# Kernel tuning notes

Measured on AMD Instinct MI355X. Metric: run time of the kernel, lower is better.

## Reference

```python
import jax, jax.numpy as jnp
import numpy as np
from jax import lax

IN_PLANES = 64
OUT_PLANES = 128
NSAMPLE = 16
BN_EPS = 1e-5


def setup_inputs() -> dict:
    key = jax.random.key(0)
    k1, k2, k3 = jax.random.split(key, 3)
    B, N = 8, 8192
    xyz = jax.random.normal(k1, (B, N, 3), jnp.float32)
    feature = jax.random.normal(k2, (B, N, IN_PLANES), jnp.float32)
    W = jax.random.normal(k3, (OUT_PLANES, IN_PLANES), jnp.float32) * (1.0 / np.sqrt(IN_PLANES))
    gamma = jnp.ones((OUT_PLANES,), jnp.float32)
    beta = jnp.zeros((OUT_PLANES,), jnp.float32)
    return {"xyz": xyz, "feature": feature, "W": W, "gamma": gamma, "beta": beta, "npoint": 2048}


def farthest_point_sample(xyz, npoint):
    # xyz: [B, N, 3] -> centroids: [B, npoint] int32. Deterministic start at index 0
    # (torch version uses a random start; math is otherwise identical).
    B, N, _ = xyz.shape

    def step(carry, _):
        distance, farthest = carry  # [B,N], [B]
        centroid = jnp.take_along_axis(xyz, farthest[:, None, None], axis=1)  # [B,1,3]
        dist = jnp.sum((xyz - centroid) ** 2, axis=-1)  # [B,N]
        distance = jnp.minimum(distance, dist)
        new_far = jnp.argmax(distance, axis=-1).astype(jnp.int32)
        return (distance, new_far), farthest

    init = (jnp.full((B, N), 1e10, xyz.dtype), jnp.zeros((B,), jnp.int32))
    _, cents = lax.scan(step, init, None, length=npoint)  # [npoint, B]
    return cents.T  # [B, npoint]


def knn_point(nsample, xyz, new_xyz):
    # squared pairwise distances [B, M, N], then k smallest
    d = (-2.0 * jnp.einsum('bmc,bnc->bmn', new_xyz, xyz)
         + jnp.sum(new_xyz ** 2, -1)[:, :, None]
         + jnp.sum(xyz ** 2, -1)[:, None, :])
    _, idx = lax.top_k(-d, nsample)  # [B, M, nsample]
    return idx


def _forward(xyz, feature, W, gamma, beta, npoint):
    cent_idx = farthest_point_sample(xyz, npoint)  # [B, npoint]
    new_xyz = jnp.take_along_axis(xyz, cent_idx[:, :, None], axis=1)  # [B, npoint, 3]
    idx = knn_point(NSAMPLE, xyz, new_xyz)  # [B, npoint, K]
    grouped = jax.vmap(lambda f, i: f[i])(feature, idx)  # [B, npoint, K, Cin]
    h = jnp.einsum('bnkc,oc->bnko', grouped, W)  # Linear, bias=False
    # BatchNorm1d over flattened (B*npoint*K, Cout): per-channel batch stats
    m = jnp.mean(h, axis=(0, 1, 2))
    v = jnp.mean((h - m) ** 2, axis=(0, 1, 2))  # biased variance (torch normalization)
    h = (h - m) * lax.rsqrt(v + BN_EPS) * gamma + beta
    h = jax.nn.relu(h)
    new_feature = jnp.max(h, axis=2)  # max-pool over K neighbors
    return new_xyz, new_feature


def reference(xyz, feature, W, gamma, beta, npoint):
    return _forward(xyz, feature, W, gamma, beta, npoint)
```

## Files before the change

kernel.cpp:

```cpp
#include <hip/hip_runtime.h>
#include <stdint.h>

#define NPTS 8192
#define NBATCH 8
#define NPOINT 2048
#define KNN_K 16
#define CIN 64
#define COUT 128

typedef unsigned long long u64;
typedef unsigned int u32;

#define MAXU64(a, b) (((a) > (b)) ? (a) : (b))
#define MAXF64(a, b) fmax((a), (b))

__device__ __forceinline__ double wave_max_f64(double v) {
#define DPPSTEP(C)                                                             \
  {                                                                            \
    u64 k = (u64)__double_as_longlong(v);                                      \
    u32 lo = (u32)k, hi = (u32)(k >> 32);                                      \
    u32 nlo = (u32)__builtin_amdgcn_update_dpp(0, (int)lo, C, 0xf, 0xf, true); \
    u32 nhi = (u32)__builtin_amdgcn_update_dpp(0, (int)hi, C, 0xf, 0xf, true); \
    double o = __longlong_as_double((long long)(((u64)nhi << 32) | nlo));      \
    v = fmax(v, o);                                                            \
  }
  DPPSTEP(0x111)
  DPPSTEP(0x112)
  DPPSTEP(0x114)
  DPPSTEP(0x118)
  DPPSTEP(0x142)
  DPPSTEP(0x143)
#undef DPPSTEP
  return v;
}

__device__ __forceinline__ double row16_max_f64(double v) {
#define DPPSTEP(C)                                                             \
  {                                                                            \
    u64 k = (u64)__double_as_longlong(v);                                      \
    u32 lo = (u32)k, hi = (u32)(k >> 32);                                      \
    u32 nlo = (u32)__builtin_amdgcn_update_dpp(0, (int)lo, C, 0xf, 0xf, true); \
    u32 nhi = (u32)__builtin_amdgcn_update_dpp(0, (int)hi, C, 0xf, 0xf, true); \
    double o = __longlong_as_double((long long)(((u64)nhi << 32) | nlo));      \
    v = fmax(v, o);                                                            \
  }
  DPPSTEP(0x111)
  DPPSTEP(0x112)
  DPPSTEP(0x114)
  DPPSTEP(0x118)
#undef DPPSTEP
  return v;
}

__device__ __forceinline__ u64 wave_max_u64(u64 k) {
  u32 lo = (u32)k, hi = (u32)(k >> 32);
#define DPPSTEP(C)                                                             \
  {                                                                            \
    u32 nlo = (u32)__builtin_amdgcn_update_dpp(0, (int)lo, C, 0xf, 0xf, true); \
    u32 nhi = (u32)__builtin_amdgcn_update_dpp(0, (int)hi, C, 0xf, 0xf, true); \
    u64 cur = ((u64)hi << 32) | lo;                                            \
    u64 oth = ((u64)nhi << 32) | nlo;                                          \
    if (oth > cur) { hi = nhi; lo = nlo; }                                     \
  }
  DPPSTEP(0x111)
  DPPSTEP(0x112)
  DPPSTEP(0x114)
  DPPSTEP(0x118)
  DPPSTEP(0x142)
  DPPSTEP(0x143)
#undef DPPSTEP
  return ((u64)hi << 32) | lo;
}

__device__ __forceinline__ float wave_min_f32(float v) {
#define STEP(C)                                                                \
  {                                                                            \
    int o = __builtin_amdgcn_update_dpp((int)__float_as_uint(v),               \
                                        (int)__float_as_uint(v), C, 0xf, 0xf,  \
                                        false);                                \
    v = fminf(v, __uint_as_float((u32)o));                                     \
  }
  STEP(0x111) STEP(0x112) STEP(0x114) STEP(0x118) STEP(0x142) STEP(0x143)
#undef STEP
  return v;
}
__device__ __forceinline__ float wave_max_f32(float v) {
#define STEP(C)                                                                \
  {                                                                            \
    int o = __builtin_amdgcn_update_dpp((int)__float_as_uint(v),               \
                                        (int)__float_as_uint(v), C, 0xf, 0xf,  \
                                        false);                                \
    v = fmaxf(v, __uint_as_float((u32)o));                                     \
  }
  STEP(0x111) STEP(0x112) STEP(0x114) STEP(0x118) STEP(0x142) STEP(0x143)
#undef STEP
  return v;
}

__device__ __forceinline__ float bcast63(float v) {
  return __uint_as_float(
      (u32)__builtin_amdgcn_readlane((int)__float_as_uint(v), 63));
}

__global__ __launch_bounds__(1024) void fps_kernel(const float* __restrict__ xyz,
                                                   int* __restrict__ cent) {
  const int b = blockIdx.x;
  const int tid = threadIdx.x;
  const int lane = tid & 63;
  const int wid = tid >> 6;
  const float* xb = xyz + (size_t)b * NPTS * 3;

  __shared__ float X[NPTS], Y[NPTS], Z[NPTS];
  __shared__ unsigned short O[NPTS];
  __shared__ float gred[16][6];
  __shared__ int cnt16[16], base16[16], cur16[16];
  __shared__ __align__(16) u64 kbuf[2][16];

  float lx[8], ly[8], lz[8];
  float xl = 3e38f, xh = -3e38f, yl = 3e38f, yh = -3e38f, zl = 3e38f, zh = -3e38f;
#pragma unroll
  for (int j = 0; j < 8; ++j) {
    int i = tid + 1024 * j;
    float x = xb[i * 3 + 0], y = xb[i * 3 + 1], z = xb[i * 3 + 2];
    lx[j] = x; ly[j] = y; lz[j] = z;
    xl = fminf(xl, x); xh = fmaxf(xh, x);
    yl = fminf(yl, y); yh = fmaxf(yh, y);
    zl = fminf(zl, z); zh = fmaxf(zh, z);
  }
  xl = wave_min_f32(xl); xh = wave_max_f32(xh);
  yl = wave_min_f32(yl); yh = wave_max_f32(yh);
  zl = wave_min_f32(zl); zh = wave_max_f32(zh);
  if (lane == 63) {
    gred[wid][0] = xl; gred[wid][1] = xh; gred[wid][2] = yl;
    gred[wid][3] = yh; gred[wid][4] = zl; gred[wid][5] = zh;
  }
  if (tid < 16) { cnt16[tid] = 0; cur16[tid] = 0; }
  __syncthreads();
  float gx0 = gred[0][0], gx1 = gred[0][1], gy0 = gred[0][2];
  float gy1 = gred[0][3], gz0 = gred[0][4], gz1 = gred[0][5];
#pragma unroll
  for (int w = 1; w < 16; ++w) {
    gx0 = fminf(gx0, gred[w][0]); gx1 = fmaxf(gx1, gred[w][1]);
    gy0 = fminf(gy0, gred[w][2]); gy1 = fmaxf(gy1, gred[w][3]);
    gz0 = fminf(gz0, gred[w][4]); gz1 = fmaxf(gz1, gred[w][5]);
  }
  const float sx = 4.f / fmaxf((gx1 - gx0) * 1.0001f, 1e-20f);
  const float sy = 2.f / fmaxf((gy1 - gy0) * 1.0001f, 1e-20f);
  const float sz = 2.f / fmaxf((gz1 - gz0) * 1.0001f, 1e-20f);

  int bin[8];
#pragma unroll
  for (int j = 0; j < 8; ++j) {
    int qx = min(3, max(0, (int)((lx[j] - gx0) * sx)));
    int qy = min(1, max(0, (int)((ly[j] - gy0) * sy)));
    int qz = min(1, max(0, (int)((lz[j] - gz0) * sz)));
    bin[j] = (qx << 2) | (qy << 1) | qz;
    atomicAdd(&cnt16[bin[j]], 1);
  }
  __syncthreads();
  if (tid == 0) {
    int s = 0;
#pragma unroll
    for (int k = 0; k < 16; ++k) { base16[k] = s; s += cnt16[k]; }
  }
  __syncthreads();
#pragma unroll
  for (int j = 0; j < 8; ++j) {
    int i = tid + 1024 * j;
    int pos = base16[bin[j]] + atomicAdd(&cur16[bin[j]], 1);
    X[pos] = lx[j]; Y[pos] = ly[j]; Z[pos] = lz[j];
    O[pos] = (unsigned short)i;
  }
  if (tid == 0) cent[b * NPOINT] = 0;
  __syncthreads();

  float px[8], py[8], pz[8], dist[8];
  u32 klo[8];
  float bxl = 3e38f, bxh = -3e38f, byl = 3e38f, byh = -3e38f, bzl = 3e38f, bzh = -3e38f;
#pragma unroll
  for (int j = 0; j < 8; ++j) {
    int p = wid * 512 + lane + 64 * j;
    float x = X[p], y = Y[p], z = Z[p];
    u32 orig = (u32)O[p];
    px[j] = x; py[j] = y; pz[j] = z;
    dist[j] = 1e10f;
    klo[j] = ((8191u - orig) << 13) | (u32)p;
    bxl = fminf(bxl, x); bxh = fmaxf(bxh, x);
    byl = fminf(byl, y); byh = fmaxf(byh, y);
    bzl = fminf(bzl, z); bzh = fmaxf(bzh, z);
  }
  const float bx0 = bcast63(wave_min_f32(bxl)), bx1 = bcast63(wave_max_f32(bxh));
  const float by0 = bcast63(wave_min_f32(byl)), by1 = bcast63(wave_max_f32(byh));
  const float bz0 = bcast63(wave_min_f32(bzl)), bz1 = bcast63(wave_max_f32(bzh));

  float cx = xb[0], cy = xb[1], cz = xb[2];
  float dmax = 1e10f;
  double prev_wk = 0.0;

  for (int it = 1; it < NPOINT; ++it) {
    float ax = fmaxf(fmaxf(bx0 - cx, cx - bx1), 0.f);
    float ay = fmaxf(fmaxf(by0 - cy, cy - by1), 0.f);
    float az = fmaxf(fmaxf(bz0 - cz, cz - bz1), 0.f);
    float LB = ax * ax + ay * ay + az * az;
    int skip = (LB > dmax * 1.00002f) ? 1 : 0;
    skip = __builtin_amdgcn_readfirstlane(skip);
    double wk;
    if (skip) {
      wk = prev_wk;
    } else {
      double key[8];
#pragma unroll
      for (int j = 0; j < 8; ++j) {
        float dx = px[j] - cx, dy = py[j] - cy, dz = pz[j] - cz;
        float dd = dx * dx + dy * dy + dz * dz;
        float t = fminf(dist[j], dd);
        dist[j] = t;
        key[j] = __longlong_as_double(
            (long long)(((u64)__float_as_uint(t) << 32) | klo[j]));
      }
#pragma unroll
      for (int s = 1; s < 8; s <<= 1) {
#pragma unroll
        for (int j = 0; j < 8; j += 2 * s) key[j] = MAXF64(key[j], key[j + s]);
      }
      wk = wave_max_f64(key[0]);
      prev_wk = wk;
    }
    if (lane == 63) kbuf[it & 1][wid] = (u64)__double_as_longlong(wk);
    dmax = __uint_as_float((u32)__builtin_amdgcn_readlane(
        (int)(u32)(((u64)__double_as_longlong(wk)) >> 32), 63));
    __syncthreads();
    double kv = __longlong_as_double((long long)kbuf[it & 1][lane & 15]);
    kv = row16_max_f64(kv);
    u32 rlo = (u32)__builtin_amdgcn_readlane(
        (int)(u32)(u64)__double_as_longlong(kv), 15);
    u32 pos = rlo & 8191u;
    if (tid == 0) cent[b * NPOINT + it] = (int)(8191u - ((rlo >> 13) & 8191u));
    cx = X[pos]; cy = Y[pos]; cz = Z[pos];
  }
}

__global__ __launch_bounds__(256) void knn_kernel(const float* __restrict__ xyz,
                                                  const int* __restrict__ cent,
                                                  int* __restrict__ knn,
                                                  float* __restrict__ out_xyz) {
  const int pt = blockIdx.x;
  const int b = pt >> 11;
  const int tid = threadIdx.x;
  const float* xb = xyz + (size_t)b * NPTS * 3;
  const int ci = cent[pt];
  const float mx = xb[ci * 3 + 0], my = xb[ci * 3 + 1], mz = xb[ci * 3 + 2];
  if (tid < 3) out_xyz[pt * 3 + tid] = xb[ci * 3 + tid];
  const float sm = mx * mx + my * my + mz * mz;

  float d[32];
  float lv = 3.0e38f;
  int lj = 0;
#pragma unroll
  for (int j = 0; j < 32; ++j) {
    int i = tid + 256 * j;
    float x = xb[i * 3 + 0], y = xb[i * 3 + 1], z = xb[i * 3 + 2];
    float dot = mx * x + my * y + mz * z;
    float sp = x * x + y * y + z * z;
    float dd = -2.0f * dot + sm + sp;
    d[j] = dd;
    if (dd < lv) { lv = dd; lj = j; }
  }

  __shared__ __align__(16) u64 kbuf[2][4];
  const int lane = tid & 63;

  for (int p = 0; p < KNN_K; ++p) {
    u32 fb = __float_as_uint(lv);
    u32 mapped = (fb & 0x80000000u) ? ~fb : (fb | 0x80000000u);
    u32 idx = (u32)(tid + (lj << 8));
    u64 ik = ~(((u64)mapped << 32) | (u64)idx);
    u64 wk = wave_max_u64(ik);
    if (lane == 63) kbuf[p & 1][tid >> 6] = wk;
    __syncthreads();
    const ulonglong2* kb = (const ulonglong2*)&kbuf[p & 1][0];
    ulonglong2 q0 = kb[0], q1 = kb[1];
    u64 best = MAXU64(MAXU64(q0.x, q0.y), MAXU64(q1.x, q1.y));
    u32 widx = (u32)(~best);
    if (tid == 0) knn[pt * KNN_K + p] = (int)widx;
    if (tid == (int)(widx & 255u)) {
      int j0 = (int)(widx >> 8);
      float nlv = 3.0e38f;
      int nlj = 0;
#pragma unroll
      for (int j = 0; j < 32; ++j) {
        if (j == j0) d[j] = 3.0e38f;
        if (d[j] < nlv) { nlv = d[j]; nlj = j; }
      }
      lv = nlv; lj = nlj;
    }
  }
}

__global__ __launch_bounds__(256) void gemm_stats_kernel(const float* __restrict__ feat,
                                                         const float* __restrict__ W,
                                                         const int* __restrict__ knn,
                                                         float* __restrict__ part,
                                                         float* __restrict__ mxbuf,
                                                         float* __restrict__ mnbuf) {
  const int tid = threadIdx.x;
  const int o0 = (tid & 63) * 2;
  const int o1 = o0 + 1;
  const int grp = tid >> 6;
  __shared__ __align__(16) float g[128][CIN];
  __shared__ int kidx[128];
  __shared__ float sred[4][128];

  const int rowbase = blockIdx.x * 128;
  if (tid < 128) kidx[tid] = knn[rowbase + tid];

  float4 w0v[16], w1v[16];
  {
    const float4* wv0 = (const float4*)(W + (size_t)o0 * CIN);
    const float4* wv1 = (const float4*)(W + (size_t)o1 * CIN);
#pragma unroll
    for (int q = 0; q < 16; ++q) { w0v[q] = wv0[q]; w1v[q] = wv1[q]; }
  }
  __syncthreads();
#pragma unroll
  for (int s = 0; s < 8; ++s) {
    int v = tid + 256 * s;
    int row = v >> 4, q = v & 15;
    int gr = rowbase + row;
    int bb = gr >> 15;
    const float4* src = (const float4*)(feat + (size_t)(bb * NPTS + kidx[row]) * CIN);
    *((float4*)&g[row][q * 4]) = src[q];
  }
  __syncthreads();

  float s1_0 = 0.f, s2_0 = 0.f, s1_1 = 0.f, s2_1 = 0.f;
#pragma unroll
  for (int pp = 0; pp < 2; ++pp) {
    const int ptl = grp + pp * 4;
    float mx0 = -3.0e38f, mn0 = 3.0e38f, mx1 = -3.0e38f, mn1 = 3.0e38f;
#pragma unroll
    for (int k = 0; k < KNN_K; ++k) {
      const int row = ptl * 16 + k;
      float a0 = 0.f, a1 = 0.f;
#pragma unroll
      for (int q = 0; q < 16; ++q) {
        float4 a = *((const float4*)&g[row][q * 4]);
        a0 += w0v[q].x * a.x + w0v[q].y * a.y + w0v[q].z * a.z + w0v[q].w * a.w;
        a1 += w1v[q].x * a.x + w1v[q].y * a.y + w1v[q].z * a.z + w1v[q].w * a.w;
      }
      s1_0 += a0; s2_0 += a0 * a0; mx0 = fmaxf(mx0, a0); mn0 = fminf(mn0, a0);
      s1_1 += a1; s2_1 += a1 * a1; mx1 = fmaxf(mx1, a1); mn1 = fminf(mn1, a1);
    }
    const size_t pt = (size_t)blockIdx.x * 8 + ptl;
    mxbuf[pt * COUT + o0] = mx0;
    mxbuf[pt * COUT + o1] = mx1;
    mnbuf[pt * COUT + o0] = mn0;
    mnbuf[pt * COUT + o1] = mn1;
  }
  sred[grp][o0] = s1_0; sred[grp][o1] = s1_1;
  __syncthreads();
  if (tid < 128) {
    float t = sred[0][tid] + sred[1][tid] + sred[2][tid] + sred[3][tid];
    part[blockIdx.x * 256 + tid] = t;
  }
  __syncthreads();
  sred[grp][o0] = s2_0; sred[grp][o1] = s2_1;
  __syncthreads();
  if (tid < 128) {
    float t = sred[0][tid] + sred[1][tid] + sred[2][tid] + sred[3][tid];
    part[blockIdx.x * 256 + 128 + tid] = t;
  }
}

__global__ __launch_bounds__(256) void bn_reduce_kernel(const float* __restrict__ part,
                                                        const float* __restrict__ gamma,
                                                        const float* __restrict__ beta,
                                                        float* __restrict__ stats) {
  const int o = blockIdx.x;
  const int tid = threadIdx.x;
  float s1 = 0.f, s2 = 0.f;
  for (int p = tid; p < 2048; p += 256) {
    s1 += part[p * 256 + o];
    s2 += part[p * 256 + 128 + o];
  }
  __shared__ float r1[256], r2[256];
  r1[tid] = s1; r2[tid] = s2;
  __syncthreads();
  for (int s = 128; s >= 1; s >>= 1) {
    if (tid < s) { r1[tid] += r1[tid + s]; r2[tid] += r2[tid + s]; }
    __syncthreads();
  }
  if (tid == 0) {
    const float n = (float)(NBATCH * NPOINT * KNN_K);
    float mean = r1[0] / n;
    float var = r2[0] / n - mean * mean;
    float inv = rsqrtf(var + 1e-5f);
    float sc = gamma[o] * inv;
    stats[o] = sc;
    stats[128 + o] = beta[o] - mean * sc;
  }
}

__global__ __launch_bounds__(256) void finalize_kernel(float* __restrict__ out_feat,
                                                       const float* __restrict__ mnbuf,
                                                       const float* __restrict__ stats) {
  const int i = blockIdx.x * 256 + threadIdx.x;
  const int o = i & 127;
  const float sc = stats[o];
  const float sh = stats[128 + o];
  const float mx = out_feat[i];
  const float mn = mnbuf[i];
  const float sel = (sc >= 0.f) ? mx : mn;
  out_feat[i] = fmaxf(sel * sc + sh, 0.f);
}

extern "C" void kernel_launch(void* const* d_in, const int* in_sizes, int n_in,
                              void* d_out, int out_size, void* d_ws, size_t ws_size,
                              hipStream_t stream) {
  const float* xyz = (const float*)d_in[0];
  const float* feat = (const float*)d_in[1];
  const float* W = (const float*)d_in[2];
  const float* gamma = (const float*)d_in[3];
  const float* beta = (const float*)d_in[4];
  float* out = (float*)d_out;

  int* cent = (int*)d_ws;
  int* knn = cent + NBATCH * NPOINT;
  float* part = (float*)(knn + NBATCH * NPOINT * KNN_K);
  float* stats = part + 2048 * 256;
  float* mnbuf = stats + 256;

  float* out_xyz = out;
  float* out_feat = out + NBATCH * NPOINT * 3;

  hipLaunchKernelGGL(fps_kernel, dim3(NBATCH), dim3(1024), 0, stream, xyz, cent);
  hipLaunchKernelGGL(knn_kernel, dim3(NBATCH * NPOINT), dim3(256), 0, stream,
                     xyz, cent, knn, out_xyz);
  hipLaunchKernelGGL(gemm_stats_kernel, dim3(2048), dim3(256), 0, stream,
                     feat, W, knn, part, out_feat, mnbuf);
  hipLaunchKernelGGL(bn_reduce_kernel, dim3(128), dim3(256), 0, stream,
                     part, gamma, beta, stats);
  hipLaunchKernelGGL(finalize_kernel, dim3(8192), dim3(256), 0, stream,
                     out_feat, mnbuf, stats);
}
```

Measured before the change: 2.147 ms.

## Restructure FPS into 8 waves with two pruned slices each and Morton 64-bin sort

The farthest point sampling kernel now runs 512 threads (8 waves) instead of 1024, and each wave owns two 512-point slices with their own bounding boxes and cached maxima. Each slice skips its distance update when its box lower bound exceeds the slice's current max. Points are sorted into 64 Morton-ordered spatial bins instead of 16, so slices are tighter and skip more often. The cross-wave reduction reads 8 keys from shared memory with vector loads instead of a DPP row reduction. The intent is to cut per-iteration compute and barrier cost in the serial FPS loop, at the cost of more serial work per wave when slices cannot be skipped.

```diff
diff --git a/kernel.cpp b/kernel.cpp
--- a/kernel.cpp
+++ b/kernel.cpp
@@ -34,24 +34,6 @@
   return v;
 }
 
-__device__ __forceinline__ double row16_max_f64(double v) {
-#define DPPSTEP(C)                                                             \
-  {                                                                            \
-    u64 k = (u64)__double_as_longlong(v);                                      \
-    u32 lo = (u32)k, hi = (u32)(k >> 32);                                      \
-    u32 nlo = (u32)__builtin_amdgcn_update_dpp(0, (int)lo, C, 0xf, 0xf, true); \
-    u32 nhi = (u32)__builtin_amdgcn_update_dpp(0, (int)hi, C, 0xf, 0xf, true); \
-    double o = __longlong_as_double((long long)(((u64)nhi << 32) | nlo));      \
-    v = fmax(v, o);                                                            \
-  }
-  DPPSTEP(0x111)
-  DPPSTEP(0x112)
-  DPPSTEP(0x114)
-  DPPSTEP(0x118)
-#undef DPPSTEP
-  return v;
-}
-
 __device__ __forceinline__ u64 wave_max_u64(u64 k) {
   u32 lo = (u32)k, hi = (u32)(k >> 32);
 #define DPPSTEP(C)                                                             \
@@ -102,8 +84,12 @@
       (u32)__builtin_amdgcn_readlane((int)__float_as_uint(v), 63));
 }
 
-__global__ __launch_bounds__(1024) void fps_kernel(const float* __restrict__ xyz,
-                                                   int* __restrict__ cent) {
+__device__ __forceinline__ u32 sp2(u32 v) {
+  return (v & 1u) | ((v & 2u) << 2);
+}
+
+__global__ __launch_bounds__(512) void fps_kernel(const float* __restrict__ xyz,
+                                                  int* __restrict__ cent) {
   const int b = blockIdx.x;
   const int tid = threadIdx.x;
   const int lane = tid & 63;
@@ -112,15 +98,15 @@
 
   __shared__ float X[NPTS], Y[NPTS], Z[NPTS];
   __shared__ unsigned short O[NPTS];
-  __shared__ float gred[16][6];
-  __shared__ int cnt16[16], base16[16], cur16[16];
-  __shared__ __align__(16) u64 kbuf[2][16];
-
-  float lx[8], ly[8], lz[8];
+  __shared__ float gred[8][6];
+  __shared__ int cnt64[64], base64[64], cur64[64];
+  __shared__ __align__(16) u64 kbuf[2][8];
+
+  float lx[16], ly[16], lz[16];
   float xl = 3e38f, xh = -3e38f, yl = 3e38f, yh = -3e38f, zl = 3e38f, zh = -3e38f;
 #pragma unroll
-  for (int j = 0; j < 8; ++j) {
-    int i = tid + 1024 * j;
+  for (int j = 0; j < 16; ++j) {
+    int i = tid + 512 * j;
     float x = xb[i * 3 + 0], y = xb[i * 3 + 1], z = xb[i * 3 + 2];
     lx[j] = x; ly[j] = y; lz[j] = z;
     xl = fminf(xl, x); xh = fmaxf(xh, x);
@@ -134,110 +120,134 @@
     gred[wid][0] = xl; gred[wid][1] = xh; gred[wid][2] = yl;
     gred[wid][3] = yh; gred[wid][4] = zl; gred[wid][5] = zh;
   }
-  if (tid < 16) { cnt16[tid] = 0; cur16[tid] = 0; }
+  if (tid < 64) { cnt64[tid] = 0; cur64[tid] = 0; }
   __syncthreads();
   float gx0 = gred[0][0], gx1 = gred[0][1], gy0 = gred[0][2];
   float gy1 = gred[0][3], gz0 = gred[0][4], gz1 = gred[0][5];
 #pragma unroll
-  for (int w = 1; w < 16; ++w) {
+  for (int w = 1; w < 8; ++w) {
     gx0 = fminf(gx0, gred[w][0]); gx1 = fmaxf(gx1, gred[w][1]);
     gy0 = fminf(gy0, gred[w][2]); gy1 = fmaxf(gy1, gred[w][3]);
     gz0 = fminf(gz0, gred[w][4]); gz1 = fmaxf(gz1, gred[w][5]);
   }
   const float sx = 4.f / fmaxf((gx1 - gx0) * 1.0001f, 1e-20f);
-  const float sy = 2.f / fmaxf((gy1 - gy0) * 1.0001f, 1e-20f);
-  const float sz = 2.f / fmaxf((gz1 - gz0) * 1.0001f, 1e-20f);
-
-  int bin[8];
-#pragma unroll
-  for (int j = 0; j < 8; ++j) {
-    int qx = min(3, max(0, (int)((lx[j] - gx0) * sx)));
-    int qy = min(1, max(0, (int)((ly[j] - gy0) * sy)));
-    int qz = min(1, max(0, (int)((lz[j] - gz0) * sz)));
-    bin[j] = (qx << 2) | (qy << 1) | qz;
-    atomicAdd(&cnt16[bin[j]], 1);
+  const float sy = 4.f / fmaxf((gy1 - gy0) * 1.0001f, 1e-20f);
+  const float sz = 4.f / fmaxf((gz1 - gz0) * 1.0001f, 1e-20f);
+
+  int bin[16];
+#pragma unroll
+  for (int j = 0; j < 16; ++j) {
+    u32 qx = (u32)min(3, max(0, (int)((lx[j] - gx0) * sx)));
+    u32 qy = (u32)min(3, max(0, (int)((ly[j] - gy0) * sy)));
+    u32 qz = (u32)min(3, max(0, (int)((lz[j] - gz0) * sz)));
+    bin[j] = (int)((sp2(qx) << 2) | (sp2(qy) << 1) | sp2(qz));
+    atomicAdd(&cnt64[bin[j]], 1);
   }
   __syncthreads();
   if (tid == 0) {
     int s = 0;
 #pragma unroll
-    for (int k = 0; k < 16; ++k) { base16[k] = s; s += cnt16[k]; }
-  }
-  __syncthreads();
-#pragma unroll
-  for (int j = 0; j < 8; ++j) {
-    int i = tid + 1024 * j;
-    int pos = base16[bin[j]] + atomicAdd(&cur16[bin[j]], 1);
+    for (int k = 0; k < 64; ++k) { base64[k] = s; s += cnt64[k]; }
+  }
+  __syncthreads();
+#pragma unroll
+  for (int j = 0; j < 16; ++j) {
+    int i = tid + 512 * j;
+    int pos = base64[bin[j]] + atomicAdd(&cur64[bin[j]], 1);
     X[pos] = lx[j]; Y[pos] = ly[j]; Z[pos] = lz[j];
     O[pos] = (unsigned short)i;
   }
   if (tid == 0) cent[b * NPOINT] = 0;
   __syncthreads();
 
-  float px[8], py[8], pz[8], dist[8];
-  u32 klo[8];
+  float pxA[8], pyA[8], pzA[8], dA[8];
+  float pxB[8], pyB[8], pzB[8], dB[8];
+  u32 kA[8], kB[8];
+  float axl = 3e38f, axh = -3e38f, ayl = 3e38f, ayh = -3e38f, azl = 3e38f, azh = -3e38f;
+#pragma unroll
+  for (int j = 0; j < 8; ++j) {
+    int p = wid * 1024 + lane + 64 * j;
+    float x = X[p], y = Y[p], z = Z[p];
+    pxA[j] = x; pyA[j] = y; pzA[j] = z;
+    dA[j] = 1e10f;
+    kA[j] = ((8191u - (u32)O[p]) << 13) | (u32)p;
+    axl = fminf(axl, x); axh = fmaxf(axh, x);
+    ayl = fminf(ayl, y); ayh = fmaxf(ayh, y);
+    azl = fminf(azl, z); azh = fmaxf(azh, z);
+  }
+  const float Ax0 = bcast63(wave_min_f32(axl)), Ax1 = bcast63(wave_max_f32(axh));
+  const float Ay0 = bcast63(wave_min_f32(ayl)), Ay1 = bcast63(wave_max_f32(ayh));
+  const float Az0 = bcast63(wave_min_f32(azl)), Az1 = bcast63(wave_max_f32(azh));
   float bxl = 3e38f, bxh = -3e38f, byl = 3e38f, byh = -3e38f, bzl = 3e38f, bzh = -3e38f;
 #pragma unroll
   for (int j = 0; j < 8; ++j) {
-    int p = wid * 512 + lane + 64 * j;
+    int p = wid * 1024 + 512 + lane + 64 * j;
     float x = X[p], y = Y[p], z = Z[p];
-    u32 orig = (u32)O[p];
-    px[j] = x; py[j] = y; pz[j] = z;
-    dist[j] = 1e10f;
-    klo[j] = ((8191u - orig) << 13) | (u32)p;
+    pxB[j] = x; pyB[j] = y; pzB[j] = z;
+    dB[j] = 1e10f;
+    kB[j] = ((8191u - (u32)O[p]) << 13) | (u32)p;
     bxl = fminf(bxl, x); bxh = fmaxf(bxh, x);
     byl = fminf(byl, y); byh = fmaxf(byh, y);
     bzl = fminf(bzl, z); bzh = fmaxf(bzh, z);
   }
-  const float bx0 = bcast63(wave_min_f32(bxl)), bx1 = bcast63(wave_max_f32(bxh));
-  const float by0 = bcast63(wave_min_f32(byl)), by1 = bcast63(wave_max_f32(byh));
-  const float bz0 = bcast63(wave_min_f32(bzl)), bz1 = bcast63(wave_max_f32(bzh));
+  const float Bx0 = bcast63(wave_min_f32(bxl)), Bx1 = bcast63(wave_max_f32(bxh));
+  const float By0 = bcast63(wave_min_f32(byl)), By1 = bcast63(wave_max_f32(byh));
+  const float Bz0 = bcast63(wave_min_f32(bzl)), Bz1 = bcast63(wave_max_f32(bzh));
 
   float cx = xb[0], cy = xb[1], cz = xb[2];
-  float dmax = 1e10f;
-  double prev_wk = 0.0;
+  u64 kc0 = ((u64)__float_as_uint(1e10f) << 32);
+  u64 kc1 = kc0;
+  float dmax0 = 1e10f, dmax1 = 1e10f;
+
+#define UPDATE_SLICE(PX, PY, PZ, DD, KK, KC, DM)                               \
+  {                                                                            \
+    double key[8];                                                             \
+    _Pragma("unroll") for (int j = 0; j < 8; ++j) {                            \
+      float dx = PX[j] - cx, dy = PY[j] - cy, dz = PZ[j] - cz;                 \
+      float dd = dx * dx + dy * dy + dz * dz;     \
+      float t = fminf(DD[j], dd);                                              \
+      DD[j] = t;                                                               \
+      key[j] = __longlong_as_double(                                           \
+          (long long)(((u64)__float_as_uint(t) << 32) | KK[j]));               \
+    }                                                                          \
+    _Pragma("unroll") for (int s = 1; s < 8; s <<= 1) {                        \
+      _Pragma("unroll") for (int j = 0; j < 8; j += 2 * s)                     \
+          key[j] = MAXF64(key[j], key[j + s]);                                 \
+    }                                                                          \
+    double wk = wave_max_f64(key[0]);                                          \
+    u64 wkb = (u64)__double_as_longlong(wk);                                   \
+    u32 hi_ = (u32)__builtin_amdgcn_readlane((int)(u32)(wkb >> 32), 63);       \
+    u32 lo_ = (u32)__builtin_amdgcn_readlane((int)(u32)wkb, 63);               \
+    KC = ((u64)hi_ << 32) | lo_;                                               \
+    DM = __uint_as_float(hi_);                                                 \
+  }
 
   for (int it = 1; it < NPOINT; ++it) {
-    float ax = fmaxf(fmaxf(bx0 - cx, cx - bx1), 0.f);
-    float ay = fmaxf(fmaxf(by0 - cy, cy - by1), 0.f);
-    float az = fmaxf(fmaxf(bz0 - cz, cz - bz1), 0.f);
-    float LB = ax * ax + ay * ay + az * az;
-    int skip = (LB > dmax * 1.00002f) ? 1 : 0;
-    skip = __builtin_amdgcn_readfirstlane(skip);
-    double wk;
-    if (skip) {
-      wk = prev_wk;
-    } else {
-      double key[8];
-#pragma unroll
-      for (int j = 0; j < 8; ++j) {
-        float dx = px[j] - cx, dy = py[j] - cy, dz = pz[j] - cz;
-        float dd = dx * dx + dy * dy + dz * dz;
-        float t = fminf(dist[j], dd);
-        dist[j] = t;
-        key[j] = __longlong_as_double(
-            (long long)(((u64)__float_as_uint(t) << 32) | klo[j]));
-      }
-#pragma unroll
-      for (int s = 1; s < 8; s <<= 1) {
-#pragma unroll
-        for (int j = 0; j < 8; j += 2 * s) key[j] = MAXF64(key[j], key[j + s]);
-      }
-      wk = wave_max_f64(key[0]);
-      prev_wk = wk;
-    }
-    if (lane == 63) kbuf[it & 1][wid] = (u64)__double_as_longlong(wk);
-    dmax = __uint_as_float((u32)__builtin_amdgcn_readlane(
-        (int)(u32)(((u64)__double_as_longlong(wk)) >> 32), 63));
+    float ax = fmaxf(fmaxf(Ax0 - cx, cx - Ax1), 0.f);
+    float ay = fmaxf(fmaxf(Ay0 - cy, cy - Ay1), 0.f);
+    float az = fmaxf(fmaxf(Az0 - cz, cz - Az1), 0.f);
+    float LB0 = ax * ax + ay * ay + az * az;
+    ax = fmaxf(fmaxf(Bx0 - cx, cx - Bx1), 0.f);
+    ay = fmaxf(fmaxf(By0 - cy, cy - By1), 0.f);
+    az = fmaxf(fmaxf(Bz0 - cz, cz - Bz1), 0.f);
+    float LB1 = ax * ax + ay * ay + az * az;
+    int dirty0 = __builtin_amdgcn_readfirstlane((LB0 > dmax0 * 1.00002f) ? 0 : 1);
+    int dirty1 = __builtin_amdgcn_readfirstlane((LB1 > dmax1 * 1.00002f) ? 0 : 1);
+    if (dirty0) UPDATE_SLICE(pxA, pyA, pzA, dA, kA, kc0, dmax0);
+    if (dirty1) UPDATE_SLICE(pxB, pyB, pzB, dB, kB, kc1, dmax1);
+    if (lane == 63) kbuf[it & 1][wid] = MAXU64(kc0, kc1);
     __syncthreads();
-    double kv = __longlong_as_double((long long)kbuf[it & 1][lane & 15]);
-    kv = row16_max_f64(kv);
-    u32 rlo = (u32)__builtin_amdgcn_readlane(
-        (int)(u32)(u64)__double_as_longlong(kv), 15);
+    const double2* kb = (const double2*)&kbuf[it & 1][0];
+    double2 p0 = kb[0], p1 = kb[1], p2 = kb[2], p3 = kb[3];
+    double m0 = MAXF64(p0.x, p0.y), m1 = MAXF64(p1.x, p1.y);
+    double m2 = MAXF64(p2.x, p2.y), m3 = MAXF64(p3.x, p3.y);
+    double best = MAXF64(MAXF64(m0, m1), MAXF64(m2, m3));
+    u32 rlo = (u32)(u64)__double_as_longlong(best);
     u32 pos = rlo & 8191u;
     if (tid == 0) cent[b * NPOINT + it] = (int)(8191u - ((rlo >> 13) & 8191u));
     cx = X[pos]; cy = Y[pos]; cz = Z[pos];
   }
+#undef UPDATE_SLICE
 }
 
 __global__ __launch_bounds__(256) void knn_kernel(const float* __restrict__ xyz,
@@ -433,7 +443,7 @@
   float* out_xyz = out;
   float* out_feat = out + NBATCH * NPOINT * 3;
 
-  hipLaunchKernelGGL(fps_kernel, dim3(NBATCH), dim3(1024), 0, stream, xyz, cent);
+  hipLaunchKernelGGL(fps_kernel, dim3(NBATCH), dim3(512), 0, stream, xyz, cent);
   hipLaunchKernelGGL(knn_kernel, dim3(NBATCH * NPOINT), dim3(256), 0, stream,
                      xyz, cent, knn, out_xyz);
   hipLaunchKernelGGL(gemm_stats_kernel, dim3(2048), dim3(256), 0, stream,
```

Result: no change. 2.129 ms (-0.8%).

## Halve FPS block to 8 waves with 64-bin Morton sorting and float4 points

Applied to the files above, without the earlier changes.

The farthest-point-sampling kernel now runs 512 threads (8 waves), each holding 16 points instead of 8. Points are sorted into 64 spatial bins, using a 4x4x4 grid with Morton-style interleaving, so each wave's bounding box is tighter and whole-wave skipping happens more often. Coordinates and original indices are packed into one float4 shared array so each centroid fetch is a single load. The cross-wave reduction shrinks to 8 entries, and dmax is updated only when a wave actually recomputes. Each wave now does more serial work per iteration and uses more registers.

```diff
diff --git a/kernel.cpp b/kernel.cpp
--- a/kernel.cpp
+++ b/kernel.cpp
@@ -34,7 +34,7 @@
   return v;
 }
 
-__device__ __forceinline__ double row16_max_f64(double v) {
+__device__ __forceinline__ double row8_max_f64(double v) {
 #define DPPSTEP(C)                                                             \
   {                                                                            \
     u64 k = (u64)__double_as_longlong(v);                                      \
@@ -47,7 +47,6 @@
   DPPSTEP(0x111)
   DPPSTEP(0x112)
   DPPSTEP(0x114)
-  DPPSTEP(0x118)
 #undef DPPSTEP
   return v;
 }
@@ -102,25 +101,28 @@
       (u32)__builtin_amdgcn_readlane((int)__float_as_uint(v), 63));
 }
 
-__global__ __launch_bounds__(1024) void fps_kernel(const float* __restrict__ xyz,
-                                                   int* __restrict__ cent) {
+__device__ __forceinline__ u32 sp2(u32 v) {
+  return (v & 1u) | ((v & 2u) << 2);
+}
+
+__global__ __launch_bounds__(512) void fps_kernel(const float* __restrict__ xyz,
+                                                  int* __restrict__ cent) {
   const int b = blockIdx.x;
   const int tid = threadIdx.x;
   const int lane = tid & 63;
   const int wid = tid >> 6;
   const float* xb = xyz + (size_t)b * NPTS * 3;
 
-  __shared__ float X[NPTS], Y[NPTS], Z[NPTS];
-  __shared__ unsigned short O[NPTS];
-  __shared__ float gred[16][6];
-  __shared__ int cnt16[16], base16[16], cur16[16];
-  __shared__ __align__(16) u64 kbuf[2][16];
-
-  float lx[8], ly[8], lz[8];
+  __shared__ __align__(16) float4 XYZ4[NPTS];
+  __shared__ float gred[8][6];
+  __shared__ int cnt64[64], base64[64], cur64[64];
+  __shared__ __align__(16) double kbuf[2][8];
+
+  float lx[16], ly[16], lz[16];
   float xl = 3e38f, xh = -3e38f, yl = 3e38f, yh = -3e38f, zl = 3e38f, zh = -3e38f;
 #pragma unroll
-  for (int j = 0; j < 8; ++j) {
-    int i = tid + 1024 * j;
+  for (int j = 0; j < 16; ++j) {
+    int i = tid + 512 * j;
     float x = xb[i * 3 + 0], y = xb[i * 3 + 1], z = xb[i * 3 + 2];
     lx[j] = x; ly[j] = y; lz[j] = z;
     xl = fminf(xl, x); xh = fmaxf(xh, x);
@@ -134,64 +136,62 @@
     gred[wid][0] = xl; gred[wid][1] = xh; gred[wid][2] = yl;
     gred[wid][3] = yh; gred[wid][4] = zl; gred[wid][5] = zh;
   }
-  if (tid < 16) { cnt16[tid] = 0; cur16[tid] = 0; }
+  if (tid < 64) { cnt64[tid] = 0; cur64[tid] = 0; }
   __syncthreads();
   float gx0 = gred[0][0], gx1 = gred[0][1], gy0 = gred[0][2];
   float gy1 = gred[0][3], gz0 = gred[0][4], gz1 = gred[0][5];
 #pragma unroll
-  for (int w = 1; w < 16; ++w) {
+  for (int w = 1; w < 8; ++w) {
     gx0 = fminf(gx0, gred[w][0]); gx1 = fmaxf(gx1, gred[w][1]);
     gy0 = fminf(gy0, gred[w][2]); gy1 = fmaxf(gy1, gred[w][3]);
     gz0 = fminf(gz0, gred[w][4]); gz1 = fmaxf(gz1, gred[w][5]);
   }
   const float sx = 4.f / fmaxf((gx1 - gx0) * 1.0001f, 1e-20f);
-  const float sy = 2.f / fmaxf((gy1 - gy0) * 1.0001f, 1e-20f);
-  const float sz = 2.f / fmaxf((gz1 - gz0) * 1.0001f, 1e-20f);
-
-  int bin[8];
-#pragma unroll
-  for (int j = 0; j < 8; ++j) {
-    int qx = min(3, max(0, (int)((lx[j] - gx0) * sx)));
-    int qy = min(1, max(0, (int)((ly[j] - gy0) * sy)));
-    int qz = min(1, max(0, (int)((lz[j] - gz0) * sz)));
-    bin[j] = (qx << 2) | (qy << 1) | qz;
-    atomicAdd(&cnt16[bin[j]], 1);
+  const float sy = 4.f / fmaxf((gy1 - gy0) * 1.0001f, 1e-20f);
+  const float sz = 4.f / fmaxf((gz1 - gz0) * 1.0001f, 1e-20f);
+
+  int bin[16];
+#pragma unroll
+  for (int j = 0; j < 16; ++j) {
+    u32 qx = (u32)min(3, max(0, (int)((lx[j] - gx0) * sx)));
+    u32 qy = (u32)min(3, max(0, (int)((ly[j] - gy0) * sy)));
+    u32 qz = (u32)min(3, max(0, (int)((lz[j] - gz0) * sz)));
+    bin[j] = (int)((sp2(qx) << 2) | (sp2(qy) << 1) | sp2(qz));
+    atomicAdd(&cnt64[bin[j]], 1);
   }
   __syncthreads();
   if (tid == 0) {
     int s = 0;
 #pragma unroll
-    for (int k = 0; k < 16; ++k) { base16[k] = s; s += cnt16[k]; }
-  }
-  __syncthreads();
-#pragma unroll
-  for (int j = 0; j < 8; ++j) {
-    int i = tid + 1024 * j;
-    int pos = base16[bin[j]] + atomicAdd(&cur16[bin[j]], 1);
-    X[pos] = lx[j]; Y[pos] = ly[j]; Z[pos] = lz[j];
-    O[pos] = (unsigned short)i;
+    for (int k = 0; k < 64; ++k) { base64[k] = s; s += cnt64[k]; }
+  }
+  __syncthreads();
+#pragma unroll
+  for (int j = 0; j < 16; ++j) {
+    int i = tid + 512 * j;
+    int pos = base64[bin[j]] + atomicAdd(&cur64[bin[j]], 1);
+    XYZ4[pos] = make_float4(lx[j], ly[j], lz[j], __uint_as_float((u32)i));
   }
   if (tid == 0) cent[b * NPOINT] = 0;
   __syncthreads();
 
-  float px[8], py[8], pz[8], dist[8];
-  u32 klo[8];
-  float bxl = 3e38f, bxh = -3e38f, byl = 3e38f, byh = -3e38f, bzl = 3e38f, bzh = -3e38f;
-#pragma unroll
-  for (int j = 0; j < 8; ++j) {
-    int p = wid * 512 + lane + 64 * j;
-    float x = X[p], y = Y[p], z = Z[p];
-    u32 orig = (u32)O[p];
-    px[j] = x; py[j] = y; pz[j] = z;
+  float px[16], py[16], pz[16], dist[16];
+  u32 klo[16];
+  float axl = 3e38f, axh = -3e38f, ayl = 3e38f, ayh = -3e38f, azl = 3e38f, azh = -3e38f;
+#pragma unroll
+  for (int j = 0; j < 16; ++j) {
+    int p = wid * 1024 + lane + 64 * j;
+    float4 v = XYZ4[p];
+    px[j] = v.x; py[j] = v.y; pz[j] = v.z;
     dist[j] = 1e10f;
-    klo[j] = ((8191u - orig) << 13) | (u32)p;
-    bxl = fminf(bxl, x); bxh = fmaxf(bxh, x);
-    byl = fminf(byl, y); byh = fmaxf(byh, y);
-    bzl = fminf(bzl, z); bzh = fmaxf(bzh, z);
-  }
-  const float bx0 = bcast63(wave_min_f32(bxl)), bx1 = bcast63(wave_max_f32(bxh));
-  const float by0 = bcast63(wave_min_f32(byl)), by1 = bcast63(wave_max_f32(byh));
-  const float bz0 = bcast63(wave_min_f32(bzl)), bz1 = bcast63(wave_max_f32(bzh));
+    klo[j] = ((8191u - __float_as_uint(v.w)) << 13) | (u32)p;
+    axl = fminf(axl, v.x); axh = fmaxf(axh, v.x);
+    ayl = fminf(ayl, v.y); ayh = fmaxf(ayh, v.y);
+    azl = fminf(azl, v.z); azh = fmaxf(azh, v.z);
+  }
+  const float bx0 = bcast63(wave_min_f32(axl)), bx1 = bcast63(wave_max_f32(axh));
+  const float by0 = bcast63(wave_min_f32(ayl)), by1 = bcast63(wave_max_f32(ayh));
+  const float bz0 = bcast63(wave_min_f32(azl)), bz1 = bcast63(wave_max_f32(azh));
 
   float cx = xb[0], cy = xb[1], cz = xb[2];
   float dmax = 1e10f;
@@ -208,9 +208,9 @@
     if (skip) {
       wk = prev_wk;
     } else {
-      double key[8];
-#pragma unroll
-      for (int j = 0; j < 8; ++j) {
+      double key[16];
+#pragma unroll
+      for (int j = 0; j < 16; ++j) {
         float dx = px[j] - cx, dy = py[j] - cy, dz = pz[j] - cz;
         float dd = dx * dx + dy * dy + dz * dz;
         float t = fminf(dist[j], dd);
@@ -219,24 +219,25 @@
             (long long)(((u64)__float_as_uint(t) << 32) | klo[j]));
       }
 #pragma unroll
-      for (int s = 1; s < 8; s <<= 1) {
-#pragma unroll
-        for (int j = 0; j < 8; j += 2 * s) key[j] = MAXF64(key[j], key[j + s]);
+      for (int s = 1; s < 16; s <<= 1) {
+#pragma unroll
+        for (int j = 0; j < 16; j += 2 * s) key[j] = MAXF64(key[j], key[j + s]);
       }
       wk = wave_max_f64(key[0]);
       prev_wk = wk;
+      dmax = __uint_as_float((u32)__builtin_amdgcn_readlane(
+          (int)(u32)(((u64)__double_as_longlong(wk)) >> 32), 63));
     }
-    if (lane == 63) kbuf[it & 1][wid] = (u64)__double_as_longlong(wk);
-    dmax = __uint_as_float((u32)__builtin_amdgcn_readlane(
-        (int)(u32)(((u64)__double_as_longlong(wk)) >> 32), 63));
+    if (lane == 63) kbuf[it & 1][wid] = wk;
     __syncthreads();
-    double kv = __longlong_as_double((long long)kbuf[it & 1][lane & 15]);
-    kv = row16_max_f64(kv);
+    double kv = kbuf[it & 1][lane & 7];
+    kv = row8_max_f64(kv);
     u32 rlo = (u32)__builtin_amdgcn_readlane(
-        (int)(u32)(u64)__double_as_longlong(kv), 15);
+        (int)(u32)(u64)__double_as_longlong(kv), 7);
     u32 pos = rlo & 8191u;
     if (tid == 0) cent[b * NPOINT + it] = (int)(8191u - ((rlo >> 13) & 8191u));
-    cx = X[pos]; cy = Y[pos]; cz = Z[pos];
+    float4 c4 = XYZ4[pos];
+    cx = c4.x; cy = c4.y; cz = c4.z;
   }
 }
 
@@ -433,7 +434,7 @@
   float* out_xyz = out;
   float* out_feat = out + NBATCH * NPOINT * 3;
 
-  hipLaunchKernelGGL(fps_kernel, dim3(NBATCH), dim3(1024), 0, stream, xyz, cent);
+  hipLaunchKernelGGL(fps_kernel, dim3(NBATCH), dim3(512), 0, stream, xyz, cent);
   hipLaunchKernelGGL(knn_kernel, dim3(NBATCH * NPOINT), dim3(256), 0, stream,
                      xyz, cent, knn, out_xyz);
   hipLaunchKernelGGL(gemm_stats_kernel, dim3(2048), dim3(256), 0, stream,
```

After: 1.998 ms (median of 2 runs). -6.9%, faster.
